# Performance work log

Measured on AMD Instinct MI355X. Metric: run time of the kernel, lower is better.

The kernel has to match this reference:

```python
import jax, jax.numpy as jnp
import numpy as np

NUM_HEADS = 16
HEAD_DIM = 128
WINDOW = 512
ROPE_BASE = 10000.0


def _rope_cos_sin(seq_len):
    inv_freq = 1.0 / (ROPE_BASE ** (jnp.arange(0, HEAD_DIM, 2, dtype=jnp.float32) / HEAD_DIM))
    freqs = jnp.arange(seq_len, dtype=jnp.float32)[:, None] * inv_freq[None, :]  # (s, d/2)
    return jnp.cos(freqs), jnp.sin(freqs)


def _apply_rotary(x, cos, sin):
    # x: (b, h, s, d); cos/sin: (s, d/2). Interleaved pairs as in the torch impl.
    x1, x2 = x[..., ::2], x[..., 1::2]
    c = cos[None, None]
    s = sin[None, None]
    r1 = x1 * c - x2 * s
    r2 = x1 * s + x2 * c
    return jnp.stack([r1, r2], axis=-1).reshape(x.shape)


def setup_inputs() -> dict:
    key = jax.random.key(0)
    ks = jax.random.split(key, 5)
    dim = NUM_HEADS * HEAD_DIM
    x = jax.random.normal(ks[0], (1, 4096, dim), dtype=jnp.float32)
    std = 0.02
    Wq = jax.random.normal(ks[1], (dim, dim), dtype=jnp.float32) * std
    Wk = jax.random.normal(ks[2], (dim, dim), dtype=jnp.float32) * std
    Wv = jax.random.normal(ks[3], (dim, dim), dtype=jnp.float32) * std
    Wo = jax.random.normal(ks[4], (dim, dim), dtype=jnp.float32) * std
    return {"x": x, "Wq": Wq, "Wk": Wk, "Wv": Wv, "Wo": Wo}


def reference(x, Wq, Wk, Wv, Wo):
    b, s, dim = x.shape
    scale = HEAD_DIM ** -0.5

    def split_heads(t):
        return t.reshape(b, s, NUM_HEADS, HEAD_DIM).transpose(0, 2, 1, 3)  # b h s d

    q = split_heads(x @ Wq.T)
    k = split_heads(x @ Wk.T)
    v = split_heads(x @ Wv.T)

    cos, sin = _rope_cos_sin(s)
    q = _apply_rotary(q, cos, sin)
    k = _apply_rotary(k, cos, sin)

    scores = jnp.einsum('bhqd,bhkd->bhqk', q, k) * scale  # (b, h, s, s)
    pos = jnp.arange(s)
    i, j = pos[:, None], pos[None, :]
    mask = (j <= i) & (i - j < WINDOW)  # sliding-window causal
    scores = jnp.where(mask[None, None], scores, -jnp.inf)
    attn = jax.nn.softmax(scores, axis=-1)

    out = jnp.einsum('bhqk,bhkd->bhqd', attn, v)
    out = out.transpose(0, 2, 1, 3).reshape(b, s, dim)
    return out @ Wo.T
```

## Files before the change

### kernel.cpp

```cpp
#include <hip/hip_runtime.h>
#include <hip/hip_bf16.h>
#include <math.h>

#define DIM 2048
#define NH 16
#define HD 128
#define WIN 512

typedef __hip_bfloat16 bf16;
using frag8 = __attribute__((ext_vector_type(8))) short;
using facc4 = __attribute__((ext_vector_type(4))) float;

__device__ inline float toF(const bf16 v) { return __bfloat162float(v); }
template <typename T> __device__ inline T fromF(float v);
template <> __device__ inline float fromF<float>(float v) { return v; }
template <> __device__ inline bf16 fromF<bf16>(float v) { return __float2bfloat16(v); }

__device__ inline unsigned bfb(float x) {
    unsigned u = __float_as_uint(x);
    u += 0x7fffu + ((u >> 16) & 1u);
    return u >> 16;
}

__device__ inline uint4 pack8(const float* p) {
    const float4 v0 = *(const float4*)p;
    const float4 v1 = *(const float4*)(p + 4);
    uint4 r;
    r.x = bfb(v0.x) | (bfb(v0.y) << 16);
    r.y = bfb(v0.z) | (bfb(v0.w) << 16);
    r.z = bfb(v1.x) | (bfb(v1.y) << 16);
    r.w = bfb(v1.z) | (bfb(v1.w) << 16);
    return r;
}

__global__ __launch_bounds__(256) void cvt_f32_bf16(const float* __restrict__ src,
                                                    bf16* __restrict__ dst, int n8) {
    const int i = blockIdx.x * 256 + threadIdx.x;
    if (i < n8) ((uint4*)dst)[i] = pack8(src + (size_t)i * 8);
}

__device__ inline void gload_lds16(const bf16* g, short* l) {
    __builtin_amdgcn_global_load_lds(
        (const __attribute__((address_space(1))) unsigned int*)g,
        (__attribute__((address_space(3))) unsigned int*)l, 16, 0, 0);
}

template <typename TC, bool SPLIT>
__global__ __launch_bounds__(256) void gemm_bt_async(const bf16* __restrict__ A,
                                                     const bf16* __restrict__ B,
                                                     TC* __restrict__ C,
                                                     bf16* __restrict__ Qp,
                                                     bf16* __restrict__ Kp,
                                                     bf16* __restrict__ Vp,
                                                     int M, int N, int K) {
    __shared__ short As[128 * 32];
    __shared__ short Bs[128 * 32];
    const int tid = threadIdx.x;
    const int lane = tid & 63;
    const int w = tid >> 6;
    const int m0 = blockIdx.y * 128;
    const int n0 = blockIdx.x * 128;
    const int wm = (w >> 1) * 64;
    const int wn = (w & 1) * 64;
    const int q = lane >> 4;
    const int mr = lane & 15;

    facc4 acc[4][4];
#pragma unroll
    for (int i = 0; i < 4; ++i)
#pragma unroll
        for (int j = 0; j < 4; ++j)
#pragma unroll
            for (int r = 0; r < 4; ++r) acc[i][j][r] = 0.f;

    for (int k0 = 0; k0 < K; k0 += 32) {
        __syncthreads();
#pragma unroll
        for (int u = 0; u < 2; ++u) {
            const int c = w * 128 + u * 64 + lane;
            const int row = c >> 2, col = (c & 3) * 8;
            gload_lds16(A + (size_t)(m0 + row) * K + k0 + col, As + (w * 128 + u * 64) * 8);
            gload_lds16(B + (size_t)(n0 + row) * K + k0 + col, Bs + (w * 128 + u * 64) * 8);
        }
        __syncthreads();

        frag8 af[4], bfr[4];
#pragma unroll
        for (int i = 0; i < 4; ++i)
            af[i] = *(const frag8*)&As[(wm + 16 * i + mr) * 32 + q * 8];
#pragma unroll
        for (int j = 0; j < 4; ++j)
            bfr[j] = *(const frag8*)&Bs[(wn + 16 * j + mr) * 32 + q * 8];
#pragma unroll
        for (int i = 0; i < 4; ++i)
#pragma unroll
            for (int j = 0; j < 4; ++j)
                acc[i][j] = __builtin_amdgcn_mfma_f32_16x16x32_bf16(af[i], bfr[j], acc[i][j], 0, 0, 0);
    }

    if (SPLIT) {
        bf16* dst = (n0 < DIM) ? Qp : ((n0 < 2 * DIM) ? Kp : Vp);
        const int nb = n0 % DIM;
#pragma unroll
        for (int i = 0; i < 4; ++i)
#pragma unroll
            for (int j = 0; j < 4; ++j) {
                const int col = nb + wn + 16 * j + mr;
#pragma unroll
                for (int r = 0; r < 4; ++r) {
                    const int row = m0 + wm + 16 * i + q * 4 + r;
                    dst[(size_t)row * DIM + col] = fromF<bf16>(acc[i][j][r]);
                }
            }
    } else {
#pragma unroll
        for (int i = 0; i < 4; ++i)
#pragma unroll
            for (int j = 0; j < 4; ++j) {
                const int col = n0 + wn + 16 * j + mr;
#pragma unroll
                for (int r = 0; r < 4; ++r) {
                    const int row = m0 + wm + 16 * i + q * 4 + r;
                    C[(size_t)row * N + col] = fromF<TC>(acc[i][j][r]);
                }
            }
    }
}

__global__ void rope_qk(bf16* __restrict__ Q, bf16* __restrict__ K, int S) {
    const int p = blockIdx.x * blockDim.x + threadIdx.x;
    const int total = S * NH * (HD / 2);
    if (p >= total) return;
    const int i = p % (HD / 2);
    const int rem = p / (HD / 2);
    const int h = rem % NH;
    const int s = rem / NH;
    const float inv = powf(10000.0f, -(float)(2 * i) / (float)HD);
    const float ang = (float)s * inv;
    float sn, cs;
    sincosf(ang, &sn, &cs);
    const size_t base = (size_t)s * DIM + h * HD + 2 * i;
    const float q1 = toF(Q[base]), q2 = toF(Q[base + 1]);
    Q[base] = fromF<bf16>(q1 * cs - q2 * sn);
    Q[base + 1] = fromF<bf16>(q1 * sn + q2 * cs);
    const float k1 = toF(K[base]), k2 = toF(K[base + 1]);
    K[base] = fromF<bf16>(k1 * cs - k2 * sn);
    K[base + 1] = fromF<bf16>(k1 * sn + k2 * cs);
}

__global__ __launch_bounds__(256, 3) void flash_swa(const bf16* __restrict__ Q,
                                                    const bf16* __restrict__ K,
                                                    const bf16* __restrict__ V,
                                                    bf16* __restrict__ O, int S) {
    __shared__ __align__(16) char lds[53248];
    short* Qs = (short*)lds;
    short* Ps = (short*)lds;
    short* Ks = (short*)(lds + 17408);
    short* Vt = (short*)(lds + 34816);

    const int tid = threadIdx.x;
    const int lane = tid & 63;
    const int w = tid >> 6;
    const int q = lane >> 4;
    const int mr = lane & 15;
    const int i0 = blockIdx.x * 64;
    const int h = blockIdx.y;
    const float scale = 0.08838834764831845f;

#pragma unroll
    for (int u = 0; u < 4; ++u) {
        const int c = tid + 256 * u;
        const int row = c >> 4, col = (c & 15) * 8;
        *(uint4*)&Qs[row * 136 + col] =
            *(const uint4*)(Q + (size_t)(i0 + row) * DIM + h * HD + col);
    }
    __syncthreads();
    frag8 qf[4];
#pragma unroll
    for (int kk = 0; kk < 4; ++kk)
        qf[kk] = *(const frag8*)&Qs[(w * 16 + mr) * 136 + kk * 32 + q * 8];

    float mrow[4], lrow[4];
    facc4 oacc[8];
#pragma unroll
    for (int r = 0; r < 4; ++r) { mrow[r] = -1e30f; lrow[r] = 0.f; }
#pragma unroll
    for (int dt = 0; dt < 8; ++dt)
#pragma unroll
        for (int r = 0; r < 4; ++r) oacc[dt][r] = 0.f;

    const int t0 = (i0 >= WIN) ? 0 : (WIN - i0) / 64;
    for (int t = t0; t < 9; ++t) {
        const int jb = i0 - WIN + t * 64;
        __syncthreads();

#pragma unroll
        for (int u = 0; u < 4; ++u) {
            const int c = tid + 256 * u;
            const int row = c >> 4, col = (c & 15) * 8;
            *(uint4*)&Ks[row * 136 + col] =
                *(const uint4*)(K + (size_t)(jb + row) * DIM + h * HD + col);
        }
#pragma unroll
        for (int it = 0; it < 2; ++it) {
            const int kp = lane & 31;
            const int dc = (lane >> 5) + 2 * it + 4 * w;
            const int d0 = dc * 8;
            const bf16* vp = V + (size_t)(jb + 2 * kp) * DIM + h * HD + d0;
            const uint4 a = *(const uint4*)vp;
            const uint4 b = *(const uint4*)(vp + DIM);
            const uint aw[4] = {a.x, a.y, a.z, a.w};
            const uint bw[4] = {b.x, b.y, b.z, b.w};
#pragma unroll
            for (int e = 0; e < 8; ++e) {
                const uint lo = (aw[e >> 1] >> (16 * (e & 1))) & 0xFFFFu;
                const uint hi = (bw[e >> 1] >> (16 * (e & 1))) & 0xFFFFu;
                ((uint*)Vt)[(d0 + e) * 36 + kp] = lo | (hi << 16);
            }
        }
        __syncthreads();

        facc4 sacc[4];
#pragma unroll
        for (int nt = 0; nt < 4; ++nt) {
#pragma unroll
            for (int r = 0; r < 4; ++r) sacc[nt][r] = 0.f;
#pragma unroll
            for (int kk = 0; kk < 4; ++kk) {
                const frag8 kfr = *(const frag8*)&Ks[(nt * 16 + mr) * 136 + kk * 32 + q * 8];
                sacc[nt] = __builtin_amdgcn_mfma_f32_16x16x32_bf16(qf[kk], kfr, sacc[nt], 0, 0, 0);
            }
        }

        float sv[4][4];
        float rmax[4] = {-1e30f, -1e30f, -1e30f, -1e30f};
#pragma unroll
        for (int nt = 0; nt < 4; ++nt) {
            const int j = jb + nt * 16 + mr;
#pragma unroll
            for (int r = 0; r < 4; ++r) {
                const int i = i0 + w * 16 + q * 4 + r;
                const bool valid = (j <= i) && (i - j < WIN);
                sv[nt][r] = valid ? sacc[nt][r] * scale : -1e30f;
                rmax[r] = fmaxf(rmax[r], sv[nt][r]);
            }
        }
#pragma unroll
        for (int msk = 1; msk <= 8; msk <<= 1)
#pragma unroll
            for (int r = 0; r < 4; ++r)
                rmax[r] = fmaxf(rmax[r], __shfl_xor(rmax[r], msk, 64));

        float alpha[4], rsum[4];
#pragma unroll
        for (int r = 0; r < 4; ++r) {
            const float mn = fmaxf(mrow[r], rmax[r]);
            alpha[r] = __expf(mrow[r] - mn);
            mrow[r] = mn;
            rsum[r] = 0.f;
        }
#pragma unroll
        for (int nt = 0; nt < 4; ++nt)
#pragma unroll
            for (int r = 0; r < 4; ++r) {
                const float pv = (sv[nt][r] > -1e29f) ? __expf(sv[nt][r] - mrow[r]) : 0.f;
                rsum[r] += pv;
                Ps[(w * 16 + q * 4 + r) * 72 + nt * 16 + mr] = (short)bfb(pv);
            }
#pragma unroll
        for (int msk = 1; msk <= 8; msk <<= 1)
#pragma unroll
            for (int r = 0; r < 4; ++r)
                rsum[r] += __shfl_xor(rsum[r], msk, 64);
#pragma unroll
        for (int r = 0; r < 4; ++r) lrow[r] = lrow[r] * alpha[r] + rsum[r];
#pragma unroll
        for (int dt = 0; dt < 8; ++dt)
#pragma unroll
            for (int r = 0; r < 4; ++r) oacc[dt][r] *= alpha[r];

        __syncthreads();

#pragma unroll
        for (int ks = 0; ks < 2; ++ks) {
            const frag8 pf = *(const frag8*)&Ps[(w * 16 + mr) * 72 + ks * 32 + q * 8];
#pragma unroll
            for (int dt = 0; dt < 8; ++dt) {
                const frag8 vf = *(const frag8*)&Vt[(dt * 16 + mr) * 72 + ks * 32 + q * 8];
                oacc[dt] = __builtin_amdgcn_mfma_f32_16x16x32_bf16(pf, vf, oacc[dt], 0, 0, 0);
            }
        }
    }

    float inv[4];
#pragma unroll
    for (int r = 0; r < 4; ++r) inv[r] = 1.0f / lrow[r];
#pragma unroll
    for (int dt = 0; dt < 8; ++dt)
#pragma unroll
        for (int r = 0; r < 4; ++r) {
            const int row = i0 + w * 16 + q * 4 + r;
            O[(size_t)row * DIM + h * HD + dt * 16 + mr] = fromF<bf16>(oacc[dt][r] * inv[r]);
        }
}

extern "C" void kernel_launch(void* const* d_in, const int* in_sizes, int n_in,
                              void* d_out, int out_size, void* d_ws, size_t ws_size,
                              hipStream_t stream) {
    const float* x  = (const float*)d_in[0];
    const float* Wq = (const float*)d_in[1];
    const float* Wk = (const float*)d_in[2];
    const float* Wv = (const float*)d_in[3];
    const float* Wo = (const float*)d_in[4];
    float* out = (float*)d_out;

    const int S = in_sizes[0] / DIM;
    const size_t elems = (size_t)S * DIM;
    const size_t wsz = (size_t)DIM * DIM;

    bf16* Q    = (bf16*)d_ws;
    bf16* K    = Q + elems;
    bf16* V    = K + elems;
    bf16* Aat  = V + elems;
    bf16* xb   = Aat + elems;
    bf16* Wcat = xb + elems;
    bf16* Wob  = Wcat + 3 * wsz;

    cvt_f32_bf16<<<(int)(elems / 8 / 256), 256, 0, stream>>>(x, xb, (int)(elems / 8));
    cvt_f32_bf16<<<(int)(wsz / 8 / 256), 256, 0, stream>>>(Wq, Wcat, (int)(wsz / 8));
    cvt_f32_bf16<<<(int)(wsz / 8 / 256), 256, 0, stream>>>(Wk, Wcat + wsz, (int)(wsz / 8));
    cvt_f32_bf16<<<(int)(wsz / 8 / 256), 256, 0, stream>>>(Wv, Wcat + 2 * wsz, (int)(wsz / 8));
    cvt_f32_bf16<<<(int)(wsz / 8 / 256), 256, 0, stream>>>(Wo, Wob, (int)(wsz / 8));

    gemm_bt_async<bf16, true><<<dim3(3 * DIM / 128, S / 128), 256, 0, stream>>>(
        xb, Wcat, (bf16*)nullptr, Q, K, V, S, 3 * DIM, DIM);

    const int pairs = S * NH * (HD / 2);
    rope_qk<<<(pairs + 255) / 256, 256, 0, stream>>>(Q, K, S);

    flash_swa<<<dim3(S / 64, NH), 256, 0, stream>>>(Q, K, V, Aat, S);

    gemm_bt_async<float, false><<<dim3(DIM / 128, S / 128), 256, 0, stream>>>(
        Aat, Wob, out, nullptr, nullptr, nullptr, S, DIM, DIM);
}
```

Baseline: 420.0 us.

## Vectorize RoPE and pre-transpose V into a global head-major layout

Replaces the scalar per-pair RoPE kernel with a vectorized version that rotates eight bf16 values per thread using 128-bit loads and a cheaper exp-based frequency. Adds a separate kernel that transposes V once into a per-head (d, s) layout in the reused xb buffer. Flash attention can then load V tiles with plain vector copies instead of repeating the shuffle-and-transpose for every window tile. This costs an extra kernel launch and an extra read and write of V.

After: 412.2 us. No clear change (-1.9%).

```diff
diff --git a/kernel.cpp b/kernel.cpp
--- a/kernel.cpp
+++ b/kernel.cpp
@@ -127,36 +127,77 @@
     }
 }
 
-__global__ void rope_qk(bf16* __restrict__ Q, bf16* __restrict__ K, int S) {
-    const int p = blockIdx.x * blockDim.x + threadIdx.x;
-    const int total = S * NH * (HD / 2);
-    if (p >= total) return;
-    const int i = p % (HD / 2);
-    const int rem = p / (HD / 2);
-    const int h = rem % NH;
-    const int s = rem / NH;
-    const float inv = powf(10000.0f, -(float)(2 * i) / (float)HD);
-    const float ang = (float)s * inv;
-    float sn, cs;
-    sincosf(ang, &sn, &cs);
-    const size_t base = (size_t)s * DIM + h * HD + 2 * i;
-    const float q1 = toF(Q[base]), q2 = toF(Q[base + 1]);
-    Q[base] = fromF<bf16>(q1 * cs - q2 * sn);
-    Q[base + 1] = fromF<bf16>(q1 * sn + q2 * cs);
-    const float k1 = toF(K[base]), k2 = toF(K[base + 1]);
-    K[base] = fromF<bf16>(k1 * cs - k2 * sn);
-    K[base + 1] = fromF<bf16>(k1 * sn + k2 * cs);
+__device__ inline uint rot_pair(uint wp, float c, float s) {
+    const float x1 = __uint_as_float((wp & 0xFFFFu) << 16);
+    const float x2 = __uint_as_float(wp & 0xFFFF0000u);
+    const float r1 = x1 * c - x2 * s;
+    const float r2 = x1 * s + x2 * c;
+    return bfb(r1) | (bfb(r2) << 16);
+}
+
+__global__ __launch_bounds__(256) void rope_qk_vec(bf16* __restrict__ Q,
+                                                   bf16* __restrict__ K, int S) {
+    const int p = blockIdx.x * 256 + threadIdx.x;
+    const int per_row = DIM / 8;
+    const int s = p / per_row;
+    const int off = (p % per_row) * 8;
+    const int f0 = (off & 127) >> 1;
+    float cs[4], sn[4];
+#pragma unroll
+    for (int t = 0; t < 4; ++t) {
+        const float inv = __expf(-0.14391157f * (float)(f0 + t));
+        sincosf((float)s * inv, &sn[t], &cs[t]);
+    }
+    const size_t base = (size_t)s * DIM + off;
+    uint4 qv = *(uint4*)(Q + base);
+    qv.x = rot_pair(qv.x, cs[0], sn[0]);
+    qv.y = rot_pair(qv.y, cs[1], sn[1]);
+    qv.z = rot_pair(qv.z, cs[2], sn[2]);
+    qv.w = rot_pair(qv.w, cs[3], sn[3]);
+    *(uint4*)(Q + base) = qv;
+    uint4 kv = *(uint4*)(K + base);
+    kv.x = rot_pair(kv.x, cs[0], sn[0]);
+    kv.y = rot_pair(kv.y, cs[1], sn[1]);
+    kv.z = rot_pair(kv.z, cs[2], sn[2]);
+    kv.w = rot_pair(kv.w, cs[3], sn[3]);
+    *(uint4*)(K + base) = kv;
+}
+
+__global__ __launch_bounds__(256) void transp_v(const bf16* __restrict__ V,
+                                                bf16* __restrict__ Vt, int S) {
+    const int tid = threadIdx.x;
+    const int lane = tid & 63;
+    const int w = tid >> 6;
+    const int k0 = blockIdx.x * 64;
+    const int h = blockIdx.y;
+#pragma unroll
+    for (int it = 0; it < 2; ++it) {
+        const int kp = lane & 31;
+        const int dc = (lane >> 5) + 2 * it + 4 * w;
+        const int d0 = dc * 8;
+        const bf16* vp = V + (size_t)(k0 + 2 * kp) * DIM + h * HD + d0;
+        const uint4 a = *(const uint4*)vp;
+        const uint4 b = *(const uint4*)(vp + DIM);
+        const uint aw[4] = {a.x, a.y, a.z, a.w};
+        const uint bw[4] = {b.x, b.y, b.z, b.w};
+#pragma unroll
+        for (int e = 0; e < 8; ++e) {
+            const uint lo = (aw[e >> 1] >> (16 * (e & 1))) & 0xFFFFu;
+            const uint hi = (bw[e >> 1] >> (16 * (e & 1))) & 0xFFFFu;
+            ((uint*)Vt)[((((size_t)h * HD + d0 + e) * S + k0) >> 1) + kp] = lo | (hi << 16);
+        }
+    }
 }
 
 __global__ __launch_bounds__(256, 3) void flash_swa(const bf16* __restrict__ Q,
                                                     const bf16* __restrict__ K,
-                                                    const bf16* __restrict__ V,
+                                                    const bf16* __restrict__ Vt,
                                                     bf16* __restrict__ O, int S) {
     __shared__ __align__(16) char lds[53248];
     short* Qs = (short*)lds;
     short* Ps = (short*)lds;
     short* Ks = (short*)(lds + 17408);
-    short* Vt = (short*)(lds + 34816);
+    short* VtL = (short*)(lds + 34816);
 
     const int tid = threadIdx.x;
     const int lane = tid & 63;
@@ -189,6 +230,8 @@
 #pragma unroll
         for (int r = 0; r < 4; ++r) oacc[dt][r] = 0.f;
 
+    const bf16* vtg = Vt + (size_t)h * HD * S;
+
     const int t0 = (i0 >= WIN) ? 0 : (WIN - i0) / 64;
     for (int t = t0; t < 9; ++t) {
         const int jb = i0 - WIN + t * 64;
@@ -202,21 +245,10 @@
                 *(const uint4*)(K + (size_t)(jb + row) * DIM + h * HD + col);
         }
 #pragma unroll
-        for (int it = 0; it < 2; ++it) {
-            const int kp = lane & 31;
-            const int dc = (lane >> 5) + 2 * it + 4 * w;
-            const int d0 = dc * 8;
-            const bf16* vp = V + (size_t)(jb + 2 * kp) * DIM + h * HD + d0;
-            const uint4 a = *(const uint4*)vp;
-            const uint4 b = *(const uint4*)(vp + DIM);
-            const uint aw[4] = {a.x, a.y, a.z, a.w};
-            const uint bw[4] = {b.x, b.y, b.z, b.w};
-#pragma unroll
-            for (int e = 0; e < 8; ++e) {
-                const uint lo = (aw[e >> 1] >> (16 * (e & 1))) & 0xFFFFu;
-                const uint hi = (bw[e >> 1] >> (16 * (e & 1))) & 0xFFFFu;
-                ((uint*)Vt)[(d0 + e) * 36 + kp] = lo | (hi << 16);
-            }
+        for (int u = 0; u < 4; ++u) {
+            const int c = tid + 256 * u;
+            const int d = c >> 3, k0c = (c & 7) * 8;
+            *(uint4*)&VtL[d * 72 + k0c] = *(const uint4*)(vtg + (size_t)d * S + jb + k0c);
         }
         __syncthreads();
 
@@ -286,7 +318,7 @@
             const frag8 pf = *(const frag8*)&Ps[(w * 16 + mr) * 72 + ks * 32 + q * 8];
 #pragma unroll
             for (int dt = 0; dt < 8; ++dt) {
-                const frag8 vf = *(const frag8*)&Vt[(dt * 16 + mr) * 72 + ks * 32 + q * 8];
+                const frag8 vf = *(const frag8*)&VtL[(dt * 16 + mr) * 72 + ks * 32 + q * 8];
                 oacc[dt] = __builtin_amdgcn_mfma_f32_16x16x32_bf16(pf, vf, oacc[dt], 0, 0, 0);
             }
         }
@@ -325,6 +357,7 @@
     bf16* xb   = Aat + elems;
     bf16* Wcat = xb + elems;
     bf16* Wob  = Wcat + 3 * wsz;
+    bf16* Vt   = xb;
 
     cvt_f32_bf16<<<(int)(elems / 8 / 256), 256, 0, stream>>>(x, xb, (int)(elems / 8));
     cvt_f32_bf16<<<(int)(wsz / 8 / 256), 256, 0, stream>>>(Wq, Wcat, (int)(wsz / 8));
@@ -335,10 +368,11 @@
     gemm_bt_async<bf16, true><<<dim3(3 * DIM / 128, S / 128), 256, 0, stream>>>(
         xb, Wcat, (bf16*)nullptr, Q, K, V, S, 3 * DIM, DIM);
 
-    const int pairs = S * NH * (HD / 2);
-    rope_qk<<<(pairs + 255) / 256, 256, 0, stream>>>(Q, K, S);
-
-    flash_swa<<<dim3(S / 64, NH), 256, 0, stream>>>(Q, K, V, Aat, S);
+    rope_qk_vec<<<(int)(elems / 8 / 256), 256, 0, stream>>>(Q, K, S);
+
+    transp_v<<<dim3(S / 64, NH), 256, 0, stream>>>(V, Vt, S);
+
+    flash_swa<<<dim3(S / 64, NH), 256, 0, stream>>>(Q, K, Vt, Aat, S);
 
     gemm_bt_async<float, false><<<dim3(DIM / 128, S / 128), 256, 0, stream>>>(
         Aat, Wob, out, nullptr, nullptr, nullptr, S, DIM, DIM);
```
